# Performance work log

Hardware: AMD Instinct MI355X
Metric: run time of the kernel (lower is better)

Reference implementation:

```python
import jax, jax.numpy as jnp
import numpy as np
from jax import lax

N_NEURONS = 2500
K = 50
T = 60
F = 5
H = 128
GROUP_SIZES = [800, 700, 600, 400]  # support_resistance, trend, pattern, volume
GID = jnp.asarray(np.repeat(np.arange(4), GROUP_SIZES))  # [N] specialty id per neuron
_BOUNDS = np.cumsum([0] + GROUP_SIZES)


def _lstm_layer(x, w_ih, w_hh, b_ih, b_hh):
    # x: [B,T,in]; PyTorch gate order i,f,g,o in the 4H weight rows
    B = x.shape[0]
    Hd = w_hh.shape[1]
    def step(carry, xt):
        h, c = carry
        g = xt @ w_ih.T + h @ w_hh.T + b_ih + b_hh
        i, f, gg, o = jnp.split(g, 4, axis=-1)
        c = jax.nn.sigmoid(f) * c + jax.nn.sigmoid(i) * jnp.tanh(gg)
        h = jax.nn.sigmoid(o) * jnp.tanh(c)
        return (h, c), h
    init = (jnp.zeros((B, Hd), x.dtype), jnp.zeros((B, Hd), x.dtype))
    (h, _), ys = lax.scan(step, init, jnp.swapaxes(x, 0, 1))
    return jnp.swapaxes(ys, 0, 1), h


def _forward(x, w_ih0, w_hh0, b_ih0, b_hh0, w_ih1, w_hh1, b_ih1, b_hh1,
             pw1, pb1, pw2, pb2, conn_w, sens, thr,
             iw1, ib1, iw2, ib2, iw3, ib3,
             hw_trend, hb_trend, hw_pat, hb_pat, hw_key, hb_key,
             hw_vol, hb_vol, hw_conf, hb_conf, conn_idx):
    seq, _ = _lstm_layer(x, w_ih0, w_hh0, b_ih0, b_hh0)
    _, h2 = _lstm_layer(seq, w_ih1, w_hh1, b_ih1, b_hh1)  # hidden[-1]: [B,H]
    # feature_projection: Linear->ReLU->Linear->Tanh
    base = jnp.tanh(jax.nn.relu(h2 @ pw1.T + pb1) @ pw2.T + pb2)  # [B,32]
    # broadcast base features to a per-neuron activation vector [B,N]
    reps = -(-N_NEURONS // base.shape[1])
    all_act = jnp.tile(base, (1, reps))[:, :N_NEURONS]
    # batched sparse gather + per-neuron weighted sum
    gathered = all_act[:, conn_idx]                       # [B,N,K]
    z = jnp.einsum('bnk,nk->bn', gathered, conn_w) * sens  # [B,N]
    # specialty-conditioned activation
    a = jnp.where(GID == 0, jax.nn.sigmoid(z - thr),
        jnp.where(GID == 1, jnp.tanh(z),
        jnp.where(GID == 2, jax.nn.relu(z - thr), jax.nn.sigmoid(z))))
    # integrator (dropout is eval-mode no-op)
    integ = jnp.tanh(jax.nn.relu(jax.nn.relu(a @ iw1.T + ib1) @ iw2.T + ib2) @ iw3.T + ib3)
    trend = integ @ hw_trend.T + hb_trend      # [B,3]
    pat = integ @ hw_pat.T + hb_pat            # [B,6]
    key_l = integ @ hw_key.T + hb_key          # [B,4]
    vol = integ @ hw_vol.T + hb_vol            # [B,1]
    conf = integ @ hw_conf.T + hb_conf         # [B,1]
    overall = jax.nn.sigmoid(conf)             # [B,1]
    means = jnp.stack([a[:, _BOUNDS[i]:_BOUNDS[i + 1]].mean(axis=1) for i in range(4)], axis=1)
    return jnp.concatenate([trend, pat, key_l, vol, conf, overall, means], axis=1)  # [B,20]


def setup_inputs() -> dict:
    key = jax.random.key(0)
    ks = iter(jax.random.split(key, 64))
    def rn(shape, s=0.05):
        return jax.random.normal(next(ks), shape, jnp.float32) * s
    B = 1024
    return {
        'x': jax.random.normal(next(ks), (B, T, F), jnp.float32),
        'conn_idx': jax.random.randint(next(ks), (N_NEURONS, K), 0, N_NEURONS, jnp.int32),
        'w_ih0': rn((4 * H, F)), 'w_hh0': rn((4 * H, H)),
        'b_ih0': rn((4 * H,), 0.01), 'b_hh0': rn((4 * H,), 0.01),
        'w_ih1': rn((4 * H, H)), 'w_hh1': rn((4 * H, H)),
        'b_ih1': rn((4 * H,), 0.01), 'b_hh1': rn((4 * H,), 0.01),
        'pw1': rn((64, H)), 'pb1': rn((64,), 0.01),
        'pw2': rn((32, 64)), 'pb2': rn((32,), 0.01),
        'conn_w': rn((N_NEURONS, K), 0.1),
        'sens': rn((N_NEURONS,), 0.1) + 1.0,
        'thr': rn((N_NEURONS,), 0.1) + 0.6,
        'iw1': rn((256, N_NEURONS), 0.01), 'ib1': rn((256,), 0.01),
        'iw2': rn((64, 256)), 'ib2': rn((64,), 0.01),
        'iw3': rn((32, 64)), 'ib3': rn((32,), 0.01),
        'hw_trend': rn((3, 32)), 'hb_trend': rn((3,), 0.01),
        'hw_pat': rn((6, 32)), 'hb_pat': rn((6,), 0.01),
        'hw_key': rn((4, 32)), 'hb_key': rn((4,), 0.01),
        'hw_vol': rn((1, 32)), 'hb_vol': rn((1,), 0.01),
        'hw_conf': rn((1, 32)), 'hb_conf': rn((1,), 0.01),
    }


def reference(x, conn_idx, w_ih0, w_hh0, b_ih0, b_hh0, w_ih1, w_hh1, b_ih1, b_hh1,
              pw1, pb1, pw2, pb2, conn_w, sens, thr,
              iw1, ib1, iw2, ib2, iw3, ib3,
              hw_trend, hb_trend, hw_pat, hb_pat, hw_key, hb_key,
              hw_vol, hb_vol, hw_conf, hb_conf):
    return _forward(x, w_ih0, w_hh0, b_ih0, b_hh0, w_ih1, w_hh1, b_ih1, b_hh1,
                    pw1, pb1, pw2, pb2, conn_w, sens, thr,
                    iw1, ib1, iw2, ib2, iw3, ib3,
                    hw_trend, hb_trend, hw_pat, hb_pat, hw_key, hb_key,
                    hw_vol, hb_vol, hw_conf, hb_conf, conn_idx)
```

## Files before the change

kernel.cpp:

```cpp
#include <hip/hip_runtime.h>
#include <hip/hip_bf16.h>
#include <math.h>

#define DEV __device__ __forceinline__

typedef short short8 __attribute__((ext_vector_type(8)));
typedef float f32x4  __attribute__((ext_vector_type(4)));

DEV float sigf(float x)   { return 1.0f / (1.0f + __expf(-x)); }
DEV float tanhft(float x) { return 1.0f - 2.0f / (__expf(2.0f * x) + 1.0f); }

DEV unsigned short f2bf(float f) {
    unsigned int u = __float_as_uint(f);
    unsigned int r = (u + 0x7FFFu + ((u >> 16) & 1u)) >> 16;
    return (unsigned short)r;
}
DEV float bf2f(unsigned short u) {
    return __uint_as_float(((unsigned int)u) << 16);
}

DEV void bar_lds() {
    asm volatile("s_waitcnt lgkmcnt(0)" ::: "memory");
    __builtin_amdgcn_s_barrier();
}

__global__ __launch_bounds__(256) void prep_kernel(
    const float* __restrict__ w_hh0, const float* __restrict__ w_ih1,
    const float* __restrict__ w_hh1,
    const float* __restrict__ b_ih0, const float* __restrict__ b_hh0,
    const float* __restrict__ b_ih1, const float* __restrict__ b_hh1,
    unsigned short* __restrict__ whh0h, unsigned short* __restrict__ wih1h,
    unsigned short* __restrict__ whh1h,
    float* __restrict__ bias0, float* __restrict__ bias1)
{
    int i = blockIdx.x * 256 + threadIdx.x;
    if (i < 65536) {
        whh0h[i] = f2bf(w_hh0[i]);
        wih1h[i] = f2bf(w_ih1[i]);
        whh1h[i] = f2bf(w_hh1[i]);
    } else if (i < 66048) {
        int c = i - 65536;
        bias0[c] = b_ih0[c] + b_hh0[c];
        bias1[c] = b_ih1[c] + b_hh1[c];
    }
}

__global__ __launch_bounds__(256) void prep_iw1_kernel(
    const float* __restrict__ iw1, unsigned short* __restrict__ iw1b)
{
    int i = blockIdx.x * 256 + threadIdx.x;
    if (i < 256 * 2528) {
        int row = i / 2528, k = i - row * 2528;
        iw1b[i] = (k < 2500) ? f2bf(iw1[row * 2500 + k]) : (unsigned short)0;
    }
}

__global__ __launch_bounds__(512, 2) void lstm_kernel(
    const float* __restrict__ x,
    const unsigned short* __restrict__ whh0,
    const unsigned short* __restrict__ wih1,
    const unsigned short* __restrict__ whh1,
    const float* __restrict__ wih0,
    const float* __restrict__ bias0, const float* __restrict__ bias1,
    float* __restrict__ h2out)
{
    __shared__ __align__(16) float          xs[4][304];
    __shared__ __align__(16) unsigned short h0s[2][16][136];
    __shared__ __align__(16) unsigned short h1s[2][16][136];
    __shared__ float gbuf0[4][512];
    __shared__ float gbuf1[4][512];
    __shared__ float wih0s[2560];

    const int tid = threadIdx.x;
    const int b0  = blockIdx.x * 4;
    const int l15 = tid & 15;
    const int q   = (tid >> 4) & 3;
    const int w   = tid >> 6;
    const int j   = w * 16 + l15;
    const int q8  = q * 8;
    const int r_u = tid >> 7;
    const int j_u = tid & 127;

    for (int i = tid; i < 1200; i += 512) {
        int m = i / 300, kk = i - m * 300;
        xs[m][kk] = x[(b0 + m) * 300 + kk];
    }
    for (int i = tid; i < 2560; i += 512) wih0s[i] = wih0[i];
    for (int i = tid; i < 2176; i += 512) {
        ((unsigned int*)h0s)[i] = 0u;
        ((unsigned int*)h1s)[i] = 0u;
    }

    const float ub0[4] = {bias0[j_u], bias0[128 + j_u], bias0[256 + j_u], bias0[384 + j_u]};
    const float ub1[4] = {bias1[j_u], bias1[128 + j_u], bias1[256 + j_u], bias1[384 + j_u]};

    short8 bh0[4][4], b1i[4][4];
#pragma unroll
    for (int g = 0; g < 4; ++g)
#pragma unroll
        for (int kc = 0; kc < 4; ++kc) {
            int off = (g * 128 + j) * 128 + kc * 32 + q8;
            bh0[g][kc] = *(const short8*)(whh0 + off);
            b1i[g][kc] = *(const short8*)(wih1 + off);
        }

    float c0 = 0.f, c1 = 0.f, hl = 0.f;
    __syncthreads();

    const unsigned short* wsb = whh1 + j * 128 + q8;

    for (int t = 0; t < 60; ++t) {
        const int p = t & 1;

        short8 wsv[4][4];
#pragma unroll
        for (int g = 0; g < 4; ++g) {
            wsv[g][0] = *(const short8*)(wsb + g * 16384);
            wsv[g][1] = *(const short8*)(wsb + g * 16384 + 32);
        }

        f32x4 acc[4];
#pragma unroll
        for (int g = 0; g < 4; ++g) acc[g] = (f32x4){0.f, 0.f, 0.f, 0.f};
        short8 af[4];
#pragma unroll
        for (int kc = 0; kc < 4; ++kc)
            af[kc] = *(const short8*)&h0s[p][l15][kc * 32 + q8];
#pragma unroll
        for (int kc = 0; kc < 4; ++kc)
#pragma unroll
            for (int g = 0; g < 4; ++g)
                acc[g] = __builtin_amdgcn_mfma_f32_16x16x32_bf16(af[kc], bh0[g][kc], acc[g], 0, 0, 0);

#pragma unroll
        for (int g = 0; g < 4; ++g) {
            wsv[g][2] = *(const short8*)(wsb + g * 16384 + 64);
            wsv[g][3] = *(const short8*)(wsb + g * 16384 + 96);
        }

        if (q == 0) {
#pragma unroll
            for (int g = 0; g < 4; ++g)
#pragma unroll
                for (int r = 0; r < 4; ++r)
                    gbuf0[r][g * 128 + j] = acc[g][r];
        }
        bar_lds();

        {
            const float* xr = &xs[r_u][t * 5];
            float x0 = xr[0], x1 = xr[1], x2 = xr[2], x3 = xr[3], x4 = xr[4];
            float gv[4];
#pragma unroll
            for (int g = 0; g < 4; ++g) {
                const float* wr = &wih0s[(g * 128 + j_u) * 5];
                float s = gbuf0[r_u][g * 128 + j_u] + ub0[g];
                s = fmaf(x0, wr[0], s);
                s = fmaf(x1, wr[1], s);
                s = fmaf(x2, wr[2], s);
                s = fmaf(x3, wr[3], s);
                gv[g] = fmaf(x4, wr[4], s);
            }
            c0 = sigf(gv[1]) * c0 + sigf(gv[0]) * tanhft(gv[2]);
            float h = sigf(gv[3]) * tanhft(c0);
            h0s[1 - p][r_u][j_u] = f2bf(h);
        }
        bar_lds();

#pragma unroll
        for (int g = 0; g < 4; ++g) acc[g] = (f32x4){0.f, 0.f, 0.f, 0.f};
#pragma unroll
        for (int kc = 0; kc < 4; ++kc)
            af[kc] = *(const short8*)&h0s[1 - p][l15][kc * 32 + q8];
#pragma unroll
        for (int kc = 0; kc < 4; ++kc)
#pragma unroll
            for (int g = 0; g < 4; ++g)
                acc[g] = __builtin_amdgcn_mfma_f32_16x16x32_bf16(af[kc], b1i[g][kc], acc[g], 0, 0, 0);
#pragma unroll
        for (int kc = 0; kc < 4; ++kc)
            af[kc] = *(const short8*)&h1s[p][l15][kc * 32 + q8];
#pragma unroll
        for (int kc = 0; kc < 4; ++kc)
#pragma unroll
            for (int g = 0; g < 4; ++g)
                acc[g] = __builtin_amdgcn_mfma_f32_16x16x32_bf16(af[kc], wsv[g][kc], acc[g], 0, 0, 0);

        if (q == 0) {
#pragma unroll
            for (int g = 0; g < 4; ++g)
#pragma unroll
                for (int r = 0; r < 4; ++r)
                    gbuf1[r][g * 128 + j] = acc[g][r];
        }
        bar_lds();

        {
            float gv[4];
#pragma unroll
            for (int g = 0; g < 4; ++g)
                gv[g] = gbuf1[r_u][g * 128 + j_u] + ub1[g];
            c1 = sigf(gv[1]) * c1 + sigf(gv[0]) * tanhft(gv[2]);
            float h = sigf(gv[3]) * tanhft(c1);
            h1s[1 - p][r_u][j_u] = f2bf(h);
            hl = h;
        }
    }

    h2out[(b0 + r_u) * 128 + j_u] = hl;
}

__global__ __launch_bounds__(64) void phase2_kernel(
    const float* __restrict__ h2, const float* __restrict__ pw1,
    const float* __restrict__ pb1, const float* __restrict__ pw2,
    const float* __restrict__ pb2, float* __restrict__ base)
{
    __shared__ float hs[128], p1[64];
    int b = blockIdx.x, tid = threadIdx.x;
    hs[tid] = h2[b * 128 + tid];
    hs[tid + 64] = h2[b * 128 + 64 + tid];
    __syncthreads();
    float acc = pb1[tid];
#pragma unroll 4
    for (int k = 0; k < 128; ++k) acc = fmaf(hs[k], pw1[tid * 128 + k], acc);
    p1[tid] = fmaxf(acc, 0.f);
    __syncthreads();
    if (tid < 32) {
        float a2 = pb2[tid];
#pragma unroll 4
        for (int k = 0; k < 64; ++k) a2 = fmaf(p1[k], pw2[tid * 64 + k], a2);
        base[b * 32 + tid] = tanhft(a2);
    }
}

__global__ __launch_bounds__(128) void weff_kernel(
    const int* __restrict__ conn_idx, const float* __restrict__ conn_w,
    float* __restrict__ weffT)
{
    __shared__ float s[128 * 33];
    int tid = threadIdx.x;
    int n = blockIdx.x * 128 + tid;
    float* sr = &s[tid * 33];
#pragma unroll
    for (int j = 0; j < 32; ++j) sr[j] = 0.f;
    if (n < 2500) {
        for (int k = 0; k < 50; ++k) {
            int idx = conn_idx[n * 50 + k];
            sr[idx & 31] += conn_w[n * 50 + k];
        }
        for (int j = 0; j < 32; ++j) weffT[j * 2500 + n] = sr[j];
    }
}

__global__ __launch_bounds__(256) void za_kernel(
    const float* __restrict__ base, const float* __restrict__ weffT,
    const float* __restrict__ sens, const float* __restrict__ thr,
    unsigned short* __restrict__ amat)
{
    __shared__ float bs[16][32];
    int tid = threadIdx.x;
    int bb = blockIdx.x / 10, nb = blockIdx.x % 10;
    int n = nb * 256 + tid;
    bool nv = n < 2500;
    bool pv = n < 2528;
    int nn = nv ? n : 0;
    for (int i = tid; i < 512; i += 256) bs[i >> 5][i & 31] = base[bb * 512 + i];
    __syncthreads();
    float w[32];
#pragma unroll
    for (int j = 0; j < 32; ++j) w[j] = weffT[j * 2500 + nn];
    float sn = sens[nn], tn = thr[nn];
    int g = (n < 800) ? 0 : (n < 1500) ? 1 : (n < 2100) ? 2 : 3;
#pragma unroll 2
    for (int r = 0; r < 16; ++r) {
        float z = 0.f;
#pragma unroll
        for (int j = 0; j < 32; ++j) z = fmaf(bs[r][j], w[j], z);
        z *= sn;
        float av;
        if (g == 0)      av = sigf(z - tn);
        else if (g == 1) av = tanhft(z);
        else if (g == 2) av = fmaxf(z - tn, 0.f);
        else             av = sigf(z);
        if (nv)      amat[(bb * 16 + r) * 2528 + n] = f2bf(av);
        else if (pv) amat[(bb * 16 + r) * 2528 + n] = 0;
    }
}

__global__ __launch_bounds__(128) void gemm_iw1_kernel(
    const unsigned short* __restrict__ ab, const unsigned short* __restrict__ wb,
    const float* __restrict__ ib1, float* __restrict__ t1)
{
    const int tid = threadIdx.x;
    const int wv  = tid >> 6;
    const int l15 = tid & 15, q = (tid >> 4) & 3, q8 = q * 8;
    const int row0 = blockIdx.y * 32 + wv * 16;
    const int col0 = blockIdx.x * 64;

    const unsigned short* A = ab + (row0 + l15) * 2528 + q8;
    const unsigned short* B = wb + (col0 + l15) * 2528 + q8;

    short8 a = *(const short8*)A;
    short8 b[4];
#pragma unroll
    for (int nt = 0; nt < 4; ++nt) b[nt] = *(const short8*)(B + nt * 16 * 2528);

    f32x4 acc[4];
#pragma unroll
    for (int nt = 0; nt < 4; ++nt) acc[nt] = (f32x4){0.f, 0.f, 0.f, 0.f};

    for (int c = 0; c < 79; ++c) {
        int cn = (c < 78) ? c + 1 : 78;
        short8 an = *(const short8*)(A + cn * 32);
        short8 bn[4];
#pragma unroll
        for (int nt = 0; nt < 4; ++nt)
            bn[nt] = *(const short8*)(B + nt * 16 * 2528 + cn * 32);
#pragma unroll
        for (int nt = 0; nt < 4; ++nt)
            acc[nt] = __builtin_amdgcn_mfma_f32_16x16x32_bf16(a, b[nt], acc[nt], 0, 0, 0);
        a = an;
#pragma unroll
        for (int nt = 0; nt < 4; ++nt) b[nt] = bn[nt];
    }

#pragma unroll
    for (int nt = 0; nt < 4; ++nt) {
        int n = col0 + nt * 16 + l15;
        float bias = ib1[n];
#pragma unroll
        for (int i = 0; i < 4; ++i) {
            int row = row0 + q * 4 + i;
            t1[row * 256 + n] = fmaxf(acc[nt][i] + bias, 0.f);
        }
    }
}

__global__ __launch_bounds__(64) void final_kernel(
    const float* __restrict__ t1, const float* __restrict__ iw2,
    const float* __restrict__ ib2, const float* __restrict__ iw3,
    const float* __restrict__ ib3,
    const float* __restrict__ hw_trend, const float* __restrict__ hb_trend,
    const float* __restrict__ hw_pat,   const float* __restrict__ hb_pat,
    const float* __restrict__ hw_key,   const float* __restrict__ hb_key,
    const float* __restrict__ hw_vol,   const float* __restrict__ hb_vol,
    const float* __restrict__ hw_conf,  const float* __restrict__ hb_conf,
    float* __restrict__ out)
{
    __shared__ float t1s[256], t2s[64], igs[32];
    int b = blockIdx.x, tid = threadIdx.x;
#pragma unroll
    for (int i = 0; i < 4; ++i) t1s[tid + i * 64] = t1[b * 256 + tid + i * 64];
    __syncthreads();
    float acc = ib2[tid];
#pragma unroll 4
    for (int k = 0; k < 256; ++k) acc = fmaf(t1s[k], iw2[tid * 256 + k], acc);
    t2s[tid] = fmaxf(acc, 0.f);
    __syncthreads();
    if (tid < 32) {
        float a2 = ib3[tid];
#pragma unroll 4
        for (int k = 0; k < 64; ++k) a2 = fmaf(t2s[k], iw3[tid * 64 + k], a2);
        igs[tid] = tanhft(a2);
    }
    __syncthreads();
    if (tid < 15) {
        const float* w; const float* bb; int j, off;
        if (tid < 3)        { w = hw_trend; bb = hb_trend; j = tid;     off = 0; }
        else if (tid < 9)   { w = hw_pat;   bb = hb_pat;   j = tid - 3; off = 3; }
        else if (tid < 13)  { w = hw_key;   bb = hb_key;   j = tid - 9; off = 9; }
        else if (tid == 13) { w = hw_vol;   bb = hb_vol;   j = 0;       off = 13; }
        else                { w = hw_conf;  bb = hb_conf;  j = 0;       off = 14; }
        float a3 = bb[j];
#pragma unroll
        for (int k = 0; k < 32; ++k) a3 = fmaf(igs[k], w[j * 32 + k], a3);
        out[b * 20 + off + j] = a3;
        if (tid == 14) out[b * 20 + 15] = sigf(a3);
    }
}

__global__ __launch_bounds__(256) void means_kernel(
    const unsigned short* __restrict__ amat, float* __restrict__ out)
{
    __shared__ float red[256];
    int b = blockIdx.x, tid = threadIdx.x;
    float parts[4] = {0.f, 0.f, 0.f, 0.f};
    for (int n = tid; n < 2500; n += 256) {
        float v = bf2f(amat[b * 2528 + n]);
        if (n < 800)       parts[0] += v;
        else if (n < 1500) parts[1] += v;
        else if (n < 2100) parts[2] += v;
        else               parts[3] += v;
    }
    const float inv[4] = {1.f / 800.f, 1.f / 700.f, 1.f / 600.f, 1.f / 400.f};
#pragma unroll
    for (int g = 0; g < 4; ++g) {
        red[tid] = parts[g];
        __syncthreads();
        for (int s = 128; s > 0; s >>= 1) {
            if (tid < s) red[tid] += red[tid + s];
            __syncthreads();
        }
        if (tid == 0) out[b * 20 + 16 + g] = red[0] * inv[g];
        __syncthreads();
    }
}

extern "C" void kernel_launch(void* const* d_in, const int* in_sizes, int n_in,
                              void* d_out, int out_size, void* d_ws, size_t ws_size,
                              hipStream_t stream)
{
    const float* x        = (const float*)d_in[0];
    const int*   conn_idx = (const int*)  d_in[1];
    const float* w_ih0    = (const float*)d_in[2];
    const float* w_hh0    = (const float*)d_in[3];
    const float* b_ih0    = (const float*)d_in[4];
    const float* b_hh0    = (const float*)d_in[5];
    const float* w_ih1    = (const float*)d_in[6];
    const float* w_hh1    = (const float*)d_in[7];
    const float* b_ih1    = (const float*)d_in[8];
    const float* b_hh1    = (const float*)d_in[9];
    const float* pw1      = (const float*)d_in[10];
    const float* pb1      = (const float*)d_in[11];
    const float* pw2      = (const float*)d_in[12];
    const float* pb2      = (const float*)d_in[13];
    const float* conn_w   = (const float*)d_in[14];
    const float* sens     = (const float*)d_in[15];
    const float* thr      = (const float*)d_in[16];
    const float* iw1      = (const float*)d_in[17];
    const float* ib1      = (const float*)d_in[18];
    const float* iw2      = (const float*)d_in[19];
    const float* ib2      = (const float*)d_in[20];
    const float* iw3      = (const float*)d_in[21];
    const float* ib3      = (const float*)d_in[22];
    const float* hw_trend = (const float*)d_in[23];
    const float* hb_trend = (const float*)d_in[24];
    const float* hw_pat   = (const float*)d_in[25];
    const float* hb_pat   = (const float*)d_in[26];
    const float* hw_key   = (const float*)d_in[27];
    const float* hb_key   = (const float*)d_in[28];
    const float* hw_vol   = (const float*)d_in[29];
    const float* hb_vol   = (const float*)d_in[30];
    const float* hw_conf  = (const float*)d_in[31];
    const float* hb_conf  = (const float*)d_in[32];
    float* out = (float*)d_out;
    float* ws  = (float*)d_ws;

    unsigned short* whh0h = (unsigned short*)(ws);
    unsigned short* wih1h = (unsigned short*)(ws + 32768);
    unsigned short* whh1h = (unsigned short*)(ws + 65536);
    float* bias0  = ws + 98304;
    float* bias1  = ws + 98816;
    float* h2     = ws + 99328;
    float* base_  = ws + 230400;
    float* weffT  = ws + 263168;
    float* t1     = ws + 343168;
    unsigned short* iw1b   = (unsigned short*)(ws + 605312);
    unsigned short* amatbf = (unsigned short*)(ws + 928896);

    prep_kernel<<<258, 256, 0, stream>>>(w_hh0, w_ih1, w_hh1,
                                         b_ih0, b_hh0, b_ih1, b_hh1,
                                         whh0h, wih1h, whh1h, bias0, bias1);
    prep_iw1_kernel<<<2528, 256, 0, stream>>>(iw1, iw1b);
    lstm_kernel<<<256, 512, 0, stream>>>(x, whh0h, wih1h, whh1h, w_ih0,
                                         bias0, bias1, h2);
    phase2_kernel<<<1024, 64, 0, stream>>>(h2, pw1, pb1, pw2, pb2, base_);
    weff_kernel<<<20, 128, 0, stream>>>(conn_idx, conn_w, weffT);
    za_kernel<<<640, 256, 0, stream>>>(base_, weffT, sens, thr, amatbf);
    gemm_iw1_kernel<<<dim3(4, 32), 128, 0, stream>>>(amatbf, iw1b, ib1, t1);
    final_kernel<<<1024, 64, 0, stream>>>(t1, iw2, ib2, iw3, ib3,
                                          hw_trend, hb_trend, hw_pat, hb_pat,
                                          hw_key, hb_key, hw_vol, hb_vol,
                                          hw_conf, hb_conf, out);
    means_kernel<<<1024, 256, 0, stream>>>(amatbf, out);
}
```

Measured before the change: 342.7 us.

## Stage layer-1 recurrent weights in swizzled LDS and vectorize means reduction

The LSTM kernel now copies the full W_hh1 bf16 matrix into a 128KB XOR-swizzled LDS buffer once, instead of reloading it from global memory every timestep. The x staging buffer and the unused padding rows of the h buffers are dropped. Only the 4 real batch rows feed A-fragments, and the other lanes pass zeros. The means kernel switches to 8-wide vector loads and a wave-shuffle reduction. The large LDS footprint likely limits occupancy to one block per CU, where launch bounds ask for two.

```diff
diff --git a/kernel.cpp b/kernel.cpp
--- a/kernel.cpp
+++ b/kernel.cpp
@@ -64,9 +64,9 @@
     const float* __restrict__ bias0, const float* __restrict__ bias1,
     float* __restrict__ h2out)
 {
-    __shared__ __align__(16) float          xs[4][304];
-    __shared__ __align__(16) unsigned short h0s[2][16][136];
-    __shared__ __align__(16) unsigned short h1s[2][16][136];
+    __shared__ __align__(16) unsigned short whh1s[65536];
+    __shared__ __align__(16) unsigned short h0s[2][4][136];
+    __shared__ __align__(16) unsigned short h1s[2][4][136];
     __shared__ float gbuf0[4][512];
     __shared__ float gbuf1[4][512];
     __shared__ float wih0s[2560];
@@ -81,12 +81,13 @@
     const int r_u = tid >> 7;
     const int j_u = tid & 127;
 
-    for (int i = tid; i < 1200; i += 512) {
-        int m = i / 300, kk = i - m * 300;
-        xs[m][kk] = x[(b0 + m) * 300 + kk];
+    for (int i = tid; i < 8192; i += 512) {
+        int jr = i >> 4, c = i & 15;
+        short8 v = *(const short8*)(whh1 + jr * 128 + c * 8);
+        *(short8*)((char*)whh1s + jr * 256 + ((c * 16) ^ ((jr & 7) << 4))) = v;
     }
     for (int i = tid; i < 2560; i += 512) wih0s[i] = wih0[i];
-    for (int i = tid; i < 2176; i += 512) {
+    for (int i = tid; i < 544; i += 512) {
         ((unsigned int*)h0s)[i] = 0u;
         ((unsigned int*)h1s)[i] = 0u;
     }
@@ -104,38 +105,44 @@
             b1i[g][kc] = *(const short8*)(wih1 + off);
         }
 
+    const int mh  = (l15 & 4) << 4;
+    const int blo = j * 256 + ((q * 16) ^ ((l15 & 3) << 4));
+
     float c0 = 0.f, c1 = 0.f, hl = 0.f;
     __syncthreads();
-
-    const unsigned short* wsb = whh1 + j * 128 + q8;
 
     for (int t = 0; t < 60; ++t) {
         const int p = t & 1;
 
+        const float* xp = x + (b0 + r_u) * 300 + t * 5;
+        float x0 = xp[0], x1 = xp[1], x2 = xp[2], x3 = xp[3], x4 = xp[4];
+
         short8 wsv[4][4];
 #pragma unroll
         for (int g = 0; g < 4; ++g) {
-            wsv[g][0] = *(const short8*)(wsb + g * 16384);
-            wsv[g][1] = *(const short8*)(wsb + g * 16384 + 32);
+            wsv[g][0] = *(const short8*)((const char*)whh1s + g * 32768 + blo + (0   ^ mh));
+            wsv[g][1] = *(const short8*)((const char*)whh1s + g * 32768 + blo + (64  ^ mh));
         }
 
         f32x4 acc[4];
 #pragma unroll
         for (int g = 0; g < 4; ++g) acc[g] = (f32x4){0.f, 0.f, 0.f, 0.f};
-        short8 af[4];
+        short8 af[4] = {};
+        if (l15 < 4) {
+#pragma unroll
+            for (int kc = 0; kc < 4; ++kc)
+                af[kc] = *(const short8*)&h0s[p][l15][kc * 32 + q8];
+        }
 #pragma unroll
         for (int kc = 0; kc < 4; ++kc)
-            af[kc] = *(const short8*)&h0s[p][l15][kc * 32 + q8];
-#pragma unroll
-        for (int kc = 0; kc < 4; ++kc)
 #pragma unroll
             for (int g = 0; g < 4; ++g)
                 acc[g] = __builtin_amdgcn_mfma_f32_16x16x32_bf16(af[kc], bh0[g][kc], acc[g], 0, 0, 0);
 
 #pragma unroll
         for (int g = 0; g < 4; ++g) {
-            wsv[g][2] = *(const short8*)(wsb + g * 16384 + 64);
-            wsv[g][3] = *(const short8*)(wsb + g * 16384 + 96);
+            wsv[g][2] = *(const short8*)((const char*)whh1s + g * 32768 + blo + (128 ^ mh));
+            wsv[g][3] = *(const short8*)((const char*)whh1s + g * 32768 + blo + (192 ^ mh));
         }
 
         if (q == 0) {
@@ -148,8 +155,6 @@
         bar_lds();
 
         {
-            const float* xr = &xs[r_u][t * 5];
-            float x0 = xr[0], x1 = xr[1], x2 = xr[2], x3 = xr[3], x4 = xr[4];
             float gv[4];
 #pragma unroll
             for (int g = 0; g < 4; ++g) {
@@ -169,22 +174,28 @@
 
 #pragma unroll
         for (int g = 0; g < 4; ++g) acc[g] = (f32x4){0.f, 0.f, 0.f, 0.f};
+        short8 af1[4] = {};
+        if (l15 < 4) {
+#pragma unroll
+            for (int kc = 0; kc < 4; ++kc)
+                af1[kc] = *(const short8*)&h0s[1 - p][l15][kc * 32 + q8];
+        }
 #pragma unroll
         for (int kc = 0; kc < 4; ++kc)
-            af[kc] = *(const short8*)&h0s[1 - p][l15][kc * 32 + q8];
+#pragma unroll
+            for (int g = 0; g < 4; ++g)
+                acc[g] = __builtin_amdgcn_mfma_f32_16x16x32_bf16(af1[kc], b1i[g][kc], acc[g], 0, 0, 0);
+        short8 af2[4] = {};
+        if (l15 < 4) {
+#pragma unroll
+            for (int kc = 0; kc < 4; ++kc)
+                af2[kc] = *(const short8*)&h1s[p][l15][kc * 32 + q8];
+        }
 #pragma unroll
         for (int kc = 0; kc < 4; ++kc)
 #pragma unroll
             for (int g = 0; g < 4; ++g)
-                acc[g] = __builtin_amdgcn_mfma_f32_16x16x32_bf16(af[kc], b1i[g][kc], acc[g], 0, 0, 0);
-#pragma unroll
-        for (int kc = 0; kc < 4; ++kc)
-            af[kc] = *(const short8*)&h1s[p][l15][kc * 32 + q8];
-#pragma unroll
-        for (int kc = 0; kc < 4; ++kc)
-#pragma unroll
-            for (int g = 0; g < 4; ++g)
-                acc[g] = __builtin_amdgcn_mfma_f32_16x16x32_bf16(af[kc], wsv[g][kc], acc[g], 0, 0, 0);
+                acc[g] = __builtin_amdgcn_mfma_f32_16x16x32_bf16(af2[kc], wsv[g][kc], acc[g], 0, 0, 0);
 
         if (q == 0) {
 #pragma unroll
@@ -382,27 +393,34 @@
 __global__ __launch_bounds__(256) void means_kernel(
     const unsigned short* __restrict__ amat, float* __restrict__ out)
 {
-    __shared__ float red[256];
+    __shared__ float red[16];
     int b = blockIdx.x, tid = threadIdx.x;
     float parts[4] = {0.f, 0.f, 0.f, 0.f};
-    for (int n = tid; n < 2500; n += 256) {
-        float v = bf2f(amat[b * 2528 + n]);
-        if (n < 800)       parts[0] += v;
-        else if (n < 1500) parts[1] += v;
-        else if (n < 2100) parts[2] += v;
-        else               parts[3] += v;
-    }
-    const float inv[4] = {1.f / 800.f, 1.f / 700.f, 1.f / 600.f, 1.f / 400.f};
+    for (int n0 = tid * 8; n0 < 2500; n0 += 2048) {
+        short8 v = *(const short8*)(amat + b * 2528 + n0);
+#pragma unroll
+        for (int e = 0; e < 8; ++e) {
+            int n = n0 + e;
+            float f = bf2f((unsigned short)v[e]);
+            if (n < 800)       parts[0] += f;
+            else if (n < 1500) parts[1] += f;
+            else if (n < 2100) parts[2] += f;
+            else               parts[3] += f;
+        }
+    }
+    int lane = tid & 63, wv = tid >> 6;
 #pragma unroll
     for (int g = 0; g < 4; ++g) {
-        red[tid] = parts[g];
-        __syncthreads();
-        for (int s = 128; s > 0; s >>= 1) {
-            if (tid < s) red[tid] += red[tid + s];
-            __syncthreads();
-        }
-        if (tid == 0) out[b * 20 + 16 + g] = red[0] * inv[g];
-        __syncthreads();
+        float v = parts[g];
+        for (int s = 32; s > 0; s >>= 1) v += __shfl_down(v, s, 64);
+        if (lane == 0) red[wv * 4 + g] = v;
+    }
+    __syncthreads();
+    if (tid < 4) {
+        float s = red[tid] + red[4 + tid] + red[8 + tid] + red[12 + tid];
+        float invg = (tid == 0) ? (1.f / 800.f) : (tid == 1) ? (1.f / 700.f)
+                   : (tid == 2) ? (1.f / 600.f) : (1.f / 400.f);
+        out[b * 20 + 16 + tid] = s * invg;
     }
 }
 
```

Measured after the change: 357.5 us. 1.04x slower.
